# Kernel tuning notes

Hardware: AMD Instinct MI355X
Metric: run time of the kernel (lower is better)

The kernel has to match this reference:

```python
import jax, jax.numpy as jnp
import numpy as np

H, F, E = 1024, 2816, 8   # hidden_size, intermediate_size, num_local_experts
B, S = 2, 2048
TOP_K = 2


def setup_inputs() -> dict:
    key = jax.random.key(0)
    ks = jax.random.split(key, 5)
    scale = 0.02
    return {
        "hidden_states": jax.random.normal(ks[0], (B, S, H), jnp.float32),
        "gate_w": jax.random.normal(ks[1], (E, H), jnp.float32) * scale,
        "w1": jax.random.normal(ks[2], (E, F, H), jnp.float32) * scale,
        "w3": jax.random.normal(ks[3], (E, F, H), jnp.float32) * scale,
        "w2": jax.random.normal(ks[4], (E, H, F), jnp.float32) * scale,
    }


def reference(hidden_states, gate_w, w1, w3, w2):
    b, s, h = hidden_states.shape
    e = gate_w.shape[0]
    T = b * s
    x = hidden_states.reshape(T, h)                      # [T, H]
    router_logits = x @ gate_w.T                         # [T, E]
    probs = jax.nn.softmax(router_logits, axis=-1)
    topw, sel = jax.lax.top_k(probs, TOP_K)              # [T, K]
    topw = topw / jnp.sum(topw, axis=-1, keepdims=True)  # renormalize over top-k
    # dense combine weights [T, E] (equivalent to the per-expert scatter/index_add)
    comb = jnp.zeros((T, e), x.dtype).at[jnp.arange(T)[:, None], sel].add(topw)
    hidden = jax.nn.silu(jnp.einsum('th,efh->etf', x, w1)) * jnp.einsum('th,efh->etf', x, w3)
    y = jnp.einsum('etf,ehf->eth', hidden, w2)           # [E, T, H]
    out = jnp.einsum('eth,te->th', y, comb)              # weighted scatter-combine
    return out.reshape(b, s, h), router_logits
```

## Files before the change

kernel.cpp:

```cpp
#include <hip/hip_runtime.h>
#include <hip/hip_bf16.h>
#include <stdint.h>

#define T_TOK 4096
#define H_DIM 1024
#define F_DIM 2816
#define E_NUM 8

typedef __attribute__((ext_vector_type(8))) __bf16 bf16x8;
typedef __attribute__((ext_vector_type(4))) float floatx4;
typedef __attribute__((address_space(3))) char lds_char;
typedef __attribute__((address_space(1))) const char glb_char;

__device__ __forceinline__ void gload16(const void* g, void* l) {
  __builtin_amdgcn_global_load_lds((glb_char*)g, (lds_char*)l, 16, 0, 0);
}

__device__ __forceinline__ unsigned pack2bf16(float a, float b) {
  unsigned ua = __builtin_bit_cast(unsigned, a);
  unsigned ub = __builtin_bit_cast(unsigned, b);
  ua += 0x7fffu + ((ua >> 16) & 1u);
  ub += 0x7fffu + ((ub >> 16) & 1u);
  return (ua >> 16) | (ub & 0xffff0000u);
}

__device__ __forceinline__ float b2f(unsigned short u) {
  unsigned v = ((unsigned)u) << 16;
  return __builtin_bit_cast(float, v);
}

__device__ __forceinline__ int swz(int row, int colb) {
  return (row * 128 + colb) ^ ((row & 7) << 4);
}

__global__ __launch_bounds__(256) void convert_kernel(
    const float* __restrict__ src, __hip_bfloat16* __restrict__ dst,
    int nchunk8) {
  int i = blockIdx.x * blockDim.x + threadIdx.x;
  const int stride = gridDim.x * blockDim.x;
  for (; i < nchunk8; i += stride) {
    const float4* s = (const float4*)(src + (size_t)i * 8);
    float4 a = s[0], b = s[1];
    uint4 p;
    p.x = pack2bf16(a.x, a.y); p.y = pack2bf16(a.z, a.w);
    p.z = pack2bf16(b.x, b.y); p.w = pack2bf16(b.z, b.w);
    *(uint4*)((char*)dst + (size_t)i * 16) = p;
  }
}

__global__ __launch_bounds__(256) void convert_w13(
    const float* __restrict__ w1, const float* __restrict__ w3,
    __hip_bfloat16* __restrict__ wB) {
  const int e = blockIdx.y;
  const int rho = blockIdx.x * 2 + (threadIdx.x >> 7);
  const int hc = threadIdx.x & 127;
  const int f = ((rho >> 5) << 4) + (rho & 15);
  const float* src = ((rho >> 4) & 1 ? w3 : w1) +
                     ((size_t)e * F_DIM + f) * H_DIM + hc * 8;
  const float4* s = (const float4*)src;
  float4 a = s[0], b = s[1];
  uint4 p;
  p.x = pack2bf16(a.x, a.y); p.y = pack2bf16(a.z, a.w);
  p.z = pack2bf16(b.x, b.y); p.w = pack2bf16(b.z, b.w);
  *(uint4*)((char*)wB + (((size_t)e * (2 * F_DIM) + rho) * H_DIM + hc * 8) * 2)
      = p;
}

__global__ __launch_bounds__(256) void router_kernel(
    const float* __restrict__ x, const float* __restrict__ gate,
    float* __restrict__ logits_out, __hip_bfloat16* __restrict__ xb,
    int* __restrict__ counts, int* __restrict__ idx_list,
    float* __restrict__ wgt_list, int* __restrict__ meta0,
    int* __restrict__ meta1, float* __restrict__ wcomb)
{
  const int wv = threadIdx.x >> 6;
  const int lane = threadIdx.x & 63;
  const int t = blockIdx.x * 4 + wv;

  const float4* xr = (const float4*)(x + (size_t)t * H_DIM);
  const float4* g4 = (const float4*)gate;

  float acc[E_NUM];
#pragma unroll
  for (int e = 0; e < E_NUM; ++e) acc[e] = 0.f;

  unsigned* xbo = (unsigned*)(xb + (size_t)t * H_DIM);
#pragma unroll
  for (int j = 0; j < 4; ++j) {
    int i = j * 64 + lane;
    float4 xv = xr[i];
    uint2 pk;
    pk.x = pack2bf16(xv.x, xv.y);
    pk.y = pack2bf16(xv.z, xv.w);
    *(uint2*)(xbo + i * 2) = pk;
#pragma unroll
    for (int e = 0; e < E_NUM; ++e) {
      float4 gv = g4[e * 256 + i];
      acc[e] += xv.x * gv.x + xv.y * gv.y + xv.z * gv.z + xv.w * gv.w;
    }
  }
#pragma unroll
  for (int off = 32; off > 0; off >>= 1) {
#pragma unroll
    for (int e = 0; e < E_NUM; ++e) acc[e] += __shfl_xor(acc[e], off, 64);
  }

  if (lane == 0) {
#pragma unroll
    for (int e = 0; e < E_NUM; ++e) logits_out[(size_t)t * E_NUM + e] = acc[e];
    int i0 = 0; float v0 = acc[0];
#pragma unroll
    for (int e = 1; e < E_NUM; ++e) if (acc[e] > v0) { v0 = acc[e]; i0 = e; }
    int i1 = -1; float v1 = -1e30f;
#pragma unroll
    for (int e = 0; e < E_NUM; ++e)
      if (e != i0 && acc[e] > v1) { v1 = acc[e]; i1 = e; }
    float p1 = __expf(v1 - v0);
    float w0 = 1.f / (1.f + p1);
    float w1 = p1 / (1.f + p1);
    int pos0 = atomicAdd(&counts[i0], 1);
    idx_list[i0 * T_TOK + pos0] = t;
    wgt_list[i0 * T_TOK + pos0] = w0;
    int pos1 = atomicAdd(&counts[i1], 1);
    idx_list[i1 * T_TOK + pos1] = t;
    wgt_list[i1 * T_TOK + pos1] = w1;
    meta0[t] = (i0 << 16) | pos0;
    meta1[t] = (i1 << 16) | pos1;
    wcomb[t] = w0;
  }
}

__global__ void scan_kernel(const int* __restrict__ counts,
                            int* __restrict__ offsets) {
  if (threadIdx.x == 0) {
    int s = 0;
    for (int e = 0; e < E_NUM; ++e) { offsets[e] = s; s += counts[e]; }
  }
}

__global__ __launch_bounds__(512, 2) void gemm1_kernel(
    const __hip_bfloat16* __restrict__ xb,
    const __hip_bfloat16* __restrict__ wB,
    const int* __restrict__ counts, const int* __restrict__ offsets,
    const int* __restrict__ idx_list, __hip_bfloat16* __restrict__ hidden)
{
  const int e = blockIdx.z;
  const int n_e = counts[e];
  const int tm = blockIdx.y;
  if (n_e == 0 || tm * 256 >= n_e) return;
  const int tn = blockIdx.x;
  const int off_e = offsets[e];

  __shared__ char lds[131072];
  char* sA = lds;
  char* sB = lds + 65536;

  const int tid = threadIdx.x;
  const int lane = tid & 63;
  const int wv = tid >> 6;
  const int wrow = (wv >> 2) * 128;
  const int wcol = (wv & 3) * 64;
  const int csw = ((lane & 7) ^ (lane >> 3)) << 4;
  const int wvb = wv * 1024;

  size_t aoff[4];
#pragma unroll
  for (int i = 0; i < 4; ++i) {
    int r = i * 64 + wv * 8 + (lane >> 3);
    int pos = tm * 256 + r;
    int p = pos < n_e ? pos : n_e - 1;
    aoff[i] = (size_t)idx_list[e * T_TOK + p] * 2048;
  }
  const char* xbp = (const char*)xb;
  const char* wBp =
      (const char*)wB + ((size_t)e * (2 * F_DIM) + tn * 256) * 2048;
  size_t boff[4];
#pragma unroll
  for (int i = 0; i < 4; ++i)
    boff[i] = (size_t)(i * 64 + wv * 8 + (lane >> 3)) * 2048;

  floatx4 acc[8][4];
#pragma unroll
  for (int m = 0; m < 8; ++m)
#pragma unroll
    for (int n = 0; n < 4; ++n)
#pragma unroll
      for (int r = 0; r < 4; ++r) acc[m][n][r] = 0.f;

#define STAGE1(set, kb)                                                \
  do {                                                                 \
    char* dA = sA + (set) * 32768 + wvb;                               \
    char* dB = sB + (set) * 32768 + wvb;                               \
    _Pragma("unroll")                                                  \
    for (int i = 0; i < 4; ++i) {                                      \
      gload16(xbp + aoff[i] + (kb) + csw, dA + i * 8192);              \
      gload16(wBp + boff[i] + (kb) + csw, dB + i * 8192);              \
    }                                                                  \
  } while (0)

  asm volatile("s_waitcnt vmcnt(0)" ::: "memory");
  STAGE1(0, 0);

  int cur = 0;
  for (int kt = 0; kt < H_DIM / 64; ++kt) {
    if (kt < H_DIM / 64 - 1) {
      STAGE1(cur ^ 1, (kt + 1) * 128);
      asm volatile("s_waitcnt vmcnt(8)" ::: "memory");
    } else {
      asm volatile("s_waitcnt vmcnt(0)" ::: "memory");
    }
    __syncthreads();
    const char* rA = sA + cur * 32768;
    const char* rB = sB + cur * 32768;
#pragma unroll
    for (int kk = 0; kk < 2; ++kk) {
      const int colb = kk * 64 + (lane >> 4) * 16;
      bf16x8 af[8], bx[4];
#pragma unroll
      for (int m = 0; m < 8; ++m)
        af[m] = *(const bf16x8*)(rA + swz(wrow + m * 16 + (lane & 15), colb));
#pragma unroll
      for (int n = 0; n < 4; ++n)
        bx[n] = *(const bf16x8*)(rB + swz(wcol + n * 16 + (lane & 15), colb));
#pragma unroll
      for (int m = 0; m < 8; ++m)
#pragma unroll
        for (int n = 0; n < 4; ++n)
          acc[m][n] = __builtin_amdgcn_mfma_f32_16x16x32_bf16(
              af[m], bx[n], acc[m][n], 0, 0, 0);
    }
    __syncthreads();
    cur ^= 1;
  }
#undef STAGE1

  const int fbase = (tn * 8 + (wcol >> 5)) * 16 + (lane & 15);
#pragma unroll
  for (int m = 0; m < 8; ++m) {
#pragma unroll
    for (int r = 0; r < 4; ++r) {
      int pos = tm * 256 + wrow + m * 16 + ((lane >> 4) << 2) + r;
      if (pos < n_e) {
        __hip_bfloat16* hrow = hidden + (size_t)(off_e + pos) * F_DIM;
#pragma unroll
        for (int j = 0; j < 2; ++j) {
          float h1 = acc[m][2 * j][r];
          float h3 = acc[m][2 * j + 1][r];
          float h = (h1 / (1.f + __expf(-h1))) * h3;
          hrow[fbase + j * 16] = __float2bfloat16(h);
        }
      }
    }
  }
}

__global__ __launch_bounds__(256, 2) void gemm2_kernel(
    const __hip_bfloat16* __restrict__ hidden,
    const __hip_bfloat16* __restrict__ w2b,
    const int* __restrict__ counts, const int* __restrict__ offsets,
    __hip_bfloat16* __restrict__ y)
{
  const int e = blockIdx.z;
  const int n_e = counts[e];
  const int tm = blockIdx.y;
  if (n_e == 0 || tm * 128 >= n_e) return;
  const int tn = blockIdx.x;
  const int n0 = tn * 128;
  const int off_e = offsets[e];

  __shared__ char lds[65536];
  char* sA = lds;
  char* sB = lds + 32768;

  const int tid = threadIdx.x;
  const int lane = tid & 63;
  const int wv = tid >> 6;
  const int wrow = (wv >> 1) * 64;
  const int wcol = (wv & 1) * 64;
  const int csw = ((lane & 7) ^ (lane >> 3)) << 4;
  const int wvb = wv * 1024;

  size_t aoff[4], boff[4];
#pragma unroll
  for (int i = 0; i < 4; ++i) {
    int r = i * 32 + wv * 8 + (lane >> 3);
    int pos = tm * 128 + r;
    int p = pos < n_e ? pos : n_e - 1;
    aoff[i] = (size_t)(off_e + p) * (F_DIM * 2);
    boff[i] = ((size_t)e * H_DIM + n0 + r) * (F_DIM * 2);
  }
  const char* hp = (const char*)hidden;
  const char* w2p = (const char*)w2b;

  floatx4 acc[4][4];
#pragma unroll
  for (int m = 0; m < 4; ++m)
#pragma unroll
    for (int n = 0; n < 4; ++n)
#pragma unroll
      for (int r = 0; r < 4; ++r) acc[m][n][r] = 0.f;

#define STAGE2(set, kb)                                                \
  do {                                                                 \
    char* dA = sA + (set) * 16384 + wvb;                               \
    char* dB = sB + (set) * 16384 + wvb;                               \
    _Pragma("unroll")                                                  \
    for (int i = 0; i < 4; ++i) {                                      \
      gload16(hp + aoff[i] + (kb) + csw, dA + i * 4096);               \
      gload16(w2p + boff[i] + (kb) + csw, dB + i * 4096);              \
    }                                                                  \
  } while (0)

  asm volatile("s_waitcnt vmcnt(0)" ::: "memory");
  STAGE2(0, 0);

  int cur = 0;
  for (int kt = 0; kt < F_DIM / 64; ++kt) {
    if (kt < F_DIM / 64 - 1) {
      STAGE2(cur ^ 1, (kt + 1) * 128);
      asm volatile("s_waitcnt vmcnt(8)" ::: "memory");
    } else {
      asm volatile("s_waitcnt vmcnt(0)" ::: "memory");
    }
    __syncthreads();
    const char* rA = sA + cur * 16384;
    const char* rB = sB + cur * 16384;
#pragma unroll
    for (int kk = 0; kk < 2; ++kk) {
      const int colb = kk * 64 + (lane >> 4) * 16;
      bf16x8 af[4], bx[4];
#pragma unroll
      for (int m = 0; m < 4; ++m)
        af[m] = *(const bf16x8*)(rA + swz(wrow + m * 16 + (lane & 15), colb));
#pragma unroll
      for (int n = 0; n < 4; ++n)
        bx[n] = *(const bf16x8*)(rB + swz(wcol + n * 16 + (lane & 15), colb));
#pragma unroll
      for (int m = 0; m < 4; ++m)
#pragma unroll
        for (int n = 0; n < 4; ++n)
          acc[m][n] = __builtin_amdgcn_mfma_f32_16x16x32_bf16(
              af[m], bx[n], acc[m][n], 0, 0, 0);
    }
    __syncthreads();
    cur ^= 1;
  }
#undef STAGE2

#pragma unroll
  for (int m = 0; m < 4; ++m) {
#pragma unroll
    for (int r = 0; r < 4; ++r) {
      int pos = tm * 128 + wrow + m * 16 + ((lane >> 4) << 2) + r;
      if (pos < n_e) {
        __hip_bfloat16* yrow = y + (size_t)(off_e + pos) * H_DIM + n0;
#pragma unroll
        for (int n = 0; n < 4; ++n)
          yrow[wcol + n * 16 + (lane & 15)] = __float2bfloat16(acc[m][n][r]);
      }
    }
  }
}

__global__ __launch_bounds__(256) void combine_kernel(
    const __hip_bfloat16* __restrict__ y, const int* __restrict__ offsets,
    const int* __restrict__ meta0, const int* __restrict__ meta1,
    const float* __restrict__ wcomb, float* __restrict__ out)
{
  const int t = blockIdx.x;
  const int m0 = meta0[t], m1 = meta1[t];
  const float w0 = wcomb[t];
  const float w1 = 1.f - w0;
  const size_t s0 = (size_t)(offsets[m0 >> 16] + (m0 & 0xffff)) * H_DIM;
  const size_t s1 = (size_t)(offsets[m1 >> 16] + (m1 & 0xffff)) * H_DIM;
  const int c = threadIdx.x * 4;
  ushort4 a = *(const ushort4*)(y + s0 + c);
  ushort4 b = *(const ushort4*)(y + s1 + c);
  float4 o;
  o.x = w0 * b2f(a.x) + w1 * b2f(b.x);
  o.y = w0 * b2f(a.y) + w1 * b2f(b.y);
  o.z = w0 * b2f(a.z) + w1 * b2f(b.z);
  o.w = w0 * b2f(a.w) + w1 * b2f(b.w);
  *(float4*)(out + (size_t)t * H_DIM + c) = o;
}

__global__ __launch_bounds__(256) void gemm1_fb(
    const __hip_bfloat16* __restrict__ xb,
    const float* __restrict__ w1, const float* __restrict__ w3,
    const int* __restrict__ counts, const int* __restrict__ offsets,
    const int* __restrict__ idx_list, __hip_bfloat16* __restrict__ hidden)
{
  const int e = blockIdx.z;
  const int n_e = counts[e];
  const int tm = blockIdx.y;
  if (n_e == 0 || tm * 128 >= n_e) return;
  const int tn = blockIdx.x;
  const int f0 = tn * 128;
  const int off_e = offsets[e];

  __shared__ short sA[128 * 64];
  __shared__ short sB1[128 * 64];
  __shared__ short sB3[128 * 64];
  __shared__ int s_row[128];

  const int tid = threadIdx.x;
  if (tid < 128) {
    int pos = tm * 128 + tid;
    int p = pos < n_e ? pos : n_e - 1;
    s_row[tid] = idx_list[e * T_TOK + p];
  }
  const int lane = tid & 63;
  const int wv = tid >> 6;
  const int wrow = (wv >> 1) * 64;
  const int wcol = (wv & 1) * 64;
  const int cc = tid & 7;
  const int rbase = tid >> 3;

  floatx4 acc1[4][4], acc3[4][4];
#pragma unroll
  for (int m = 0; m < 4; ++m)
#pragma unroll
    for (int n = 0; n < 4; ++n)
#pragma unroll
      for (int r = 0; r < 4; ++r) { acc1[m][n][r] = 0.f; acc3[m][n][r] = 0.f; }

  const float* w1e = w1 + (size_t)e * F_DIM * H_DIM + (size_t)f0 * H_DIM;
  const float* w3e = w3 + (size_t)e * F_DIM * H_DIM + (size_t)f0 * H_DIM;

  for (int kt = 0; kt < H_DIM / 64; ++kt) {
    const int k0 = kt * 64;
    __syncthreads();
#pragma unroll
    for (int i = 0; i < 4; ++i) {
      int r = rbase + 32 * i;
      uint4 av = *(const uint4*)(xb + (size_t)s_row[r] * H_DIM + k0 + cc * 8);
      *(uint4*)((char*)sA + swz(r, cc * 16)) = av;
      const float4* p1 = (const float4*)(w1e + (size_t)r * H_DIM + k0 + cc * 8);
      float4 a1 = p1[0], b1 = p1[1];
      uint4 pb1;
      pb1.x = pack2bf16(a1.x, a1.y); pb1.y = pack2bf16(a1.z, a1.w);
      pb1.z = pack2bf16(b1.x, b1.y); pb1.w = pack2bf16(b1.z, b1.w);
      *(uint4*)((char*)sB1 + swz(r, cc * 16)) = pb1;
      const float4* p3 = (const float4*)(w3e + (size_t)r * H_DIM + k0 + cc * 8);
      float4 a3 = p3[0], b3 = p3[1];
      uint4 pb3;
      pb3.x = pack2bf16(a3.x, a3.y); pb3.y = pack2bf16(a3.z, a3.w);
      pb3.z = pack2bf16(b3.x, b3.y); pb3.w = pack2bf16(b3.z, b3.w);
      *(uint4*)((char*)sB3 + swz(r, cc * 16)) = pb3;
    }
    __syncthreads();
#pragma unroll
    for (int kk = 0; kk < 2; ++kk) {
      const int colb = kk * 64 + (lane >> 4) * 16;
      bf16x8 af[4], bf1[4], bf3[4];
#pragma unroll
      for (int m = 0; m < 4; ++m)
        af[m] = *(const bf16x8*)((const char*)sA +
                                 swz(wrow + m * 16 + (lane & 15), colb));
#pragma unroll
      for (int n = 0; n < 4; ++n) {
        bf1[n] = *(const bf16x8*)((const char*)sB1 +
                                  swz(wcol + n * 16 + (lane & 15), colb));
        bf3[n] = *(const bf16x8*)((const char*)sB3 +
                                  swz(wcol + n * 16 + (lane & 15), colb));
      }
#pragma unroll
      for (int m = 0; m < 4; ++m)
#pragma unroll
        for (int n = 0; n < 4; ++n) {
          acc1[m][n] = __builtin_amdgcn_mfma_f32_16x16x32_bf16(
              af[m], bf1[n], acc1[m][n], 0, 0, 0);
          acc3[m][n] = __builtin_amdgcn_mfma_f32_16x16x32_bf16(
              af[m], bf3[n], acc3[m][n], 0, 0, 0);
        }
    }
  }
#pragma unroll
  for (int m = 0; m < 4; ++m) {
#pragma unroll
    for (int r = 0; r < 4; ++r) {
      int rl = wrow + m * 16 + ((lane >> 4) << 2) + r;
      int pos = tm * 128 + rl;
      if (pos < n_e) {
        __hip_bfloat16* hrow = hidden + (size_t)(off_e + pos) * F_DIM + f0;
#pragma unroll
        for (int n = 0; n < 4; ++n) {
          float h1 = acc1[m][n][r];
          float h3 = acc3[m][n][r];
          float h = (h1 / (1.f + __expf(-h1))) * h3;
          hrow[wcol + n * 16 + (lane & 15)] = __float2bfloat16(h);
        }
      }
    }
  }
}

__global__ __launch_bounds__(256) void gemm2_fb(
    const __hip_bfloat16* __restrict__ hidden, const float* __restrict__ w2,
    const int* __restrict__ counts, const int* __restrict__ offsets,
    const int* __restrict__ idx_list, const float* __restrict__ wgt_list,
    float* __restrict__ out)
{
  const int e = blockIdx.z;
  const int n_e = counts[e];
  const int tm = blockIdx.y;
  if (n_e == 0 || tm * 128 >= n_e) return;
  const int tn = blockIdx.x;
  const int n0 = tn * 128;
  const int off_e = offsets[e];

  __shared__ short sA[128 * 64];
  __shared__ short sB[128 * 64];
  __shared__ int s_tok[128];
  __shared__ float s_wgt[128];

  const int tid = threadIdx.x;
  if (tid < 128) {
    int pos = tm * 128 + tid;
    if (pos < n_e) {
      s_tok[tid] = idx_list[e * T_TOK + pos];
      s_wgt[tid] = wgt_list[e * T_TOK + pos];
    } else {
      s_tok[tid] = -1;
      s_wgt[tid] = 0.f;
    }
  }
  const int lane = tid & 63;
  const int wv = tid >> 6;
  const int wrow = (wv >> 1) * 64;
  const int wcol = (wv & 1) * 64;
  const int cc = tid & 7;
  const int rbase = tid >> 3;

  floatx4 acc[4][4];
#pragma unroll
  for (int m = 0; m < 4; ++m)
#pragma unroll
    for (int n = 0; n < 4; ++n)
#pragma unroll
      for (int r = 0; r < 4; ++r) acc[m][n][r] = 0.f;

  const float* w2e = w2 + (size_t)e * H_DIM * F_DIM + (size_t)n0 * F_DIM;

  for (int kt = 0; kt < F_DIM / 64; ++kt) {
    const int k0 = kt * 64;
    __syncthreads();
#pragma unroll
    for (int i = 0; i < 4; ++i) {
      int r = rbase + 32 * i;
      int pos = tm * 128 + r;
      int pr = pos < n_e ? pos : n_e - 1;
      uint4 av = *(const uint4*)(hidden + (size_t)(off_e + pr) * F_DIM +
                                 k0 + cc * 8);
      *(uint4*)((char*)sA + swz(r, cc * 16)) = av;
      const float4* pb = (const float4*)(w2e + (size_t)r * F_DIM + k0 + cc * 8);
      float4 ba = pb[0], bb = pb[1];
      uint4 pk;
      pk.x = pack2bf16(ba.x, ba.y); pk.y = pack2bf16(ba.z, ba.w);
      pk.z = pack2bf16(bb.x, bb.y); pk.w = pack2bf16(bb.z, bb.w);
      *(uint4*)((char*)sB + swz(r, cc * 16)) = pk;
    }
    __syncthreads();
#pragma unroll
    for (int kk = 0; kk < 2; ++kk) {
      const int colb = kk * 64 + (lane >> 4) * 16;
      bf16x8 af[4], bf[4];
#pragma unroll
      for (int m = 0; m < 4; ++m)
        af[m] = *(const bf16x8*)((const char*)sA +
                                 swz(wrow + m * 16 + (lane & 15), colb));
#pragma unroll
      for (int n = 0; n < 4; ++n)
        bf[n] = *(const bf16x8*)((const char*)sB +
                                 swz(wcol + n * 16 + (lane & 15), colb));
#pragma unroll
      for (int m = 0; m < 4; ++m)
#pragma unroll
        for (int n = 0; n < 4; ++n)
          acc[m][n] = __builtin_amdgcn_mfma_f32_16x16x32_bf16(
              af[m], bf[n], acc[m][n], 0, 0, 0);
    }
  }
#pragma unroll
  for (int m = 0; m < 4; ++m) {
#pragma unroll
    for (int r = 0; r < 4; ++r) {
      int rl = wrow + m * 16 + ((lane >> 4) << 2) + r;
      int tok = s_tok[rl];
      if (tok >= 0) {
        float wgt = s_wgt[rl];
        float* orow = out + (size_t)tok * H_DIM + n0;
#pragma unroll
        for (int n = 0; n < 4; ++n)
          atomicAdd(&orow[wcol + n * 16 + (lane & 15)], wgt * acc[m][n][r]);
      }
    }
  }
}

extern "C" void kernel_launch(void* const* d_in, const int* in_sizes, int n_in,
                              void* d_out, int out_size, void* d_ws,
                              size_t ws_size, hipStream_t stream) {
  const float* x = (const float*)d_in[0];
  const float* gate = (const float*)d_in[1];
  const float* w1 = (const float*)d_in[2];
  const float* w3 = (const float*)d_in[3];
  const float* w2 = (const float*)d_in[4];

  float* out = (float*)d_out;
  float* logits = out + (size_t)T_TOK * H_DIM;

  char* ws = (char*)d_ws;
  const size_t o_idx = 256;
  const size_t o_wgt = o_idx + (size_t)E_NUM * T_TOK * 4;
  const size_t o_m0  = o_wgt + (size_t)E_NUM * T_TOK * 4;
  const size_t o_m1  = o_m0 + (size_t)T_TOK * 4;
  const size_t o_wc  = o_m1 + (size_t)T_TOK * 4;
  const size_t o_xb  = o_wc + (size_t)T_TOK * 4;
  const size_t o_hid = o_xb + (size_t)T_TOK * H_DIM * 2;
  const size_t o_wB  = o_hid + (size_t)2 * T_TOK * F_DIM * 2;
  const size_t o_w2b = o_wB + (size_t)E_NUM * 2 * F_DIM * H_DIM * 2;
  const size_t need  = o_w2b + (size_t)E_NUM * H_DIM * F_DIM * 2;

  int* counts = (int*)ws;
  int* offsets = counts + 8;
  int* idx_list = (int*)(ws + o_idx);
  float* wgt_list = (float*)(ws + o_wgt);
  int* meta0 = (int*)(ws + o_m0);
  int* meta1 = (int*)(ws + o_m1);
  float* wcomb = (float*)(ws + o_wc);
  __hip_bfloat16* xb = (__hip_bfloat16*)(ws + o_xb);
  __hip_bfloat16* hidden = (__hip_bfloat16*)(ws + o_hid);

  hipMemsetAsync(counts, 0, 64, stream);

  if (ws_size >= need) {
    __hip_bfloat16* wB = (__hip_bfloat16*)(ws + o_wB);
    __hip_bfloat16* w2b = (__hip_bfloat16*)(ws + o_w2b);
    __hip_bfloat16* y = (__hip_bfloat16*)(ws + o_wB);

    convert_w13<<<dim3(F_DIM, E_NUM), 256, 0, stream>>>(w1, w3, wB);
    convert_kernel<<<2048, 256, 0, stream>>>(
        w2, w2b, E_NUM * F_DIM * H_DIM / 8);
    router_kernel<<<T_TOK / 4, 256, 0, stream>>>(
        x, gate, logits, xb, counts, idx_list, wgt_list, meta0, meta1, wcomb);
    scan_kernel<<<1, 64, 0, stream>>>(counts, offsets);
    gemm1_kernel<<<dim3(2 * F_DIM / 256, T_TOK / 256, E_NUM), 512, 0,
                   stream>>>(xb, wB, counts, offsets, idx_list, hidden);
    gemm2_kernel<<<dim3(H_DIM / 128, T_TOK / 128, E_NUM), 256, 0, stream>>>(
        hidden, w2b, counts, offsets, y);
    combine_kernel<<<T_TOK, 256, 0, stream>>>(y, offsets, meta0, meta1, wcomb,
                                              out);
  } else {
    hipMemsetAsync(out, 0, (size_t)T_TOK * H_DIM * sizeof(float), stream);
    router_kernel<<<T_TOK / 4, 256, 0, stream>>>(
        x, gate, logits, xb, counts, idx_list, wgt_list, meta0, meta1, wcomb);
    scan_kernel<<<1, 64, 0, stream>>>(counts, offsets);
    gemm1_fb<<<dim3(F_DIM / 128, T_TOK / 128, E_NUM), 256, 0, stream>>>(
        xb, w1, w3, counts, offsets, idx_list, hidden);
    gemm2_fb<<<dim3(H_DIM / 128, T_TOK / 128, E_NUM), 256, 0, stream>>>(
        hidden, w2, counts, offsets, idx_list, wgt_list, out);
  }
}
```

Measured before the change: 446.8 us.

## Split-K gemm2 in halves and remap gemm1 block order across experts

gemm2 now splits its F reduction into two halves along a doubled grid z dimension, writing two partial y buffers that the combine kernel sums. This doubles the block count to fill the GPU better, at the cost of extra y traffic and bf16 rounding of each partial. gemm1 linearizes its block index and remaps it so that consecutive blocks hit different experts in a rotated pattern. That is meant to spread work and weight reads across experts and balance early exits. The second y half sits at an offset of 2*T*H in the workspace, which relies on the region aliased over wB being large enough.

Result: no change. 447.2 us (+0.1%).

```diff
diff --git a/kernel.cpp b/kernel.cpp
--- a/kernel.cpp
+++ b/kernel.cpp
@@ -144,11 +144,14 @@
     const int* __restrict__ counts, const int* __restrict__ offsets,
     const int* __restrict__ idx_list, __hip_bfloat16* __restrict__ hidden)
 {
-  const int e = blockIdx.z;
+  const int L = blockIdx.x + 22 * (blockIdx.y + 16 * blockIdx.z);
+  const int k = L & 7;
+  const int r = L >> 3;
+  const int tn = r >> 4;
+  const int tm = r & 15;
+  const int e = (k - tn) & 7;
   const int n_e = counts[e];
-  const int tm = blockIdx.y;
   if (n_e == 0 || tm * 256 >= n_e) return;
-  const int tn = blockIdx.x;
   const int off_e = offsets[e];
 
   __shared__ char lds[131072];
@@ -166,8 +169,8 @@
   size_t aoff[4];
 #pragma unroll
   for (int i = 0; i < 4; ++i) {
-    int r = i * 64 + wv * 8 + (lane >> 3);
-    int pos = tm * 256 + r;
+    int rr = i * 64 + wv * 8 + (lane >> 3);
+    int pos = tm * 256 + rr;
     int p = pos < n_e ? pos : n_e - 1;
     aoff[i] = (size_t)idx_list[e * T_TOK + p] * 2048;
   }
@@ -185,7 +188,7 @@
 #pragma unroll
     for (int n = 0; n < 4; ++n)
 #pragma unroll
-      for (int r = 0; r < 4; ++r) acc[m][n][r] = 0.f;
+      for (int q = 0; q < 4; ++q) acc[m][n][q] = 0.f;
 
 #define STAGE1(set, kb)                                                \
   do {                                                                 \
@@ -238,14 +241,14 @@
 #pragma unroll
   for (int m = 0; m < 8; ++m) {
 #pragma unroll
-    for (int r = 0; r < 4; ++r) {
-      int pos = tm * 256 + wrow + m * 16 + ((lane >> 4) << 2) + r;
+    for (int q = 0; q < 4; ++q) {
+      int pos = tm * 256 + wrow + m * 16 + ((lane >> 4) << 2) + q;
       if (pos < n_e) {
         __hip_bfloat16* hrow = hidden + (size_t)(off_e + pos) * F_DIM;
 #pragma unroll
         for (int j = 0; j < 2; ++j) {
-          float h1 = acc[m][2 * j][r];
-          float h3 = acc[m][2 * j + 1][r];
+          float h1 = acc[m][2 * j][q];
+          float h3 = acc[m][2 * j + 1][q];
           float h = (h1 / (1.f + __expf(-h1))) * h3;
           hrow[fbase + j * 16] = __float2bfloat16(h);
         }
@@ -260,13 +263,15 @@
     const int* __restrict__ counts, const int* __restrict__ offsets,
     __hip_bfloat16* __restrict__ y)
 {
-  const int e = blockIdx.z;
+  const int e = blockIdx.z & 7;
+  const int kh = blockIdx.z >> 3;
+  const int tm = blockIdx.y;
+  const int tn = blockIdx.x;
   const int n_e = counts[e];
-  const int tm = blockIdx.y;
   if (n_e == 0 || tm * 128 >= n_e) return;
-  const int tn = blockIdx.x;
   const int n0 = tn * 128;
   const int off_e = offsets[e];
+  const int kbase = kh * (F_DIM);
 
   __shared__ char lds[65536];
   char* sA = lds;
@@ -283,11 +288,11 @@
   size_t aoff[4], boff[4];
 #pragma unroll
   for (int i = 0; i < 4; ++i) {
-    int r = i * 32 + wv * 8 + (lane >> 3);
-    int pos = tm * 128 + r;
+    int rr = i * 32 + wv * 8 + (lane >> 3);
+    int pos = tm * 128 + rr;
     int p = pos < n_e ? pos : n_e - 1;
     aoff[i] = (size_t)(off_e + p) * (F_DIM * 2);
-    boff[i] = ((size_t)e * H_DIM + n0 + r) * (F_DIM * 2);
+    boff[i] = ((size_t)e * H_DIM + n0 + rr) * (F_DIM * 2);
   }
   const char* hp = (const char*)hidden;
   const char* w2p = (const char*)w2b;
@@ -298,7 +303,7 @@
 #pragma unroll
     for (int n = 0; n < 4; ++n)
 #pragma unroll
-      for (int r = 0; r < 4; ++r) acc[m][n][r] = 0.f;
+      for (int q = 0; q < 4; ++q) acc[m][n][q] = 0.f;
 
 #define STAGE2(set, kb)                                                \
   do {                                                                 \
@@ -312,12 +317,13 @@
   } while (0)
 
   asm volatile("s_waitcnt vmcnt(0)" ::: "memory");
-  STAGE2(0, 0);
+  STAGE2(0, kbase);
 
   int cur = 0;
-  for (int kt = 0; kt < F_DIM / 64; ++kt) {
-    if (kt < F_DIM / 64 - 1) {
-      STAGE2(cur ^ 1, (kt + 1) * 128);
+  const int NKT = F_DIM / 64 / 2;
+  for (int kt = 0; kt < NKT; ++kt) {
+    if (kt < NKT - 1) {
+      STAGE2(cur ^ 1, kbase + (kt + 1) * 128);
       asm volatile("s_waitcnt vmcnt(8)" ::: "memory");
     } else {
       asm volatile("s_waitcnt vmcnt(0)" ::: "memory");
@@ -347,16 +353,17 @@
   }
 #undef STAGE2
 
+  __hip_bfloat16* yh = y + (size_t)kh * (2 * T_TOK) * H_DIM;
 #pragma unroll
   for (int m = 0; m < 4; ++m) {
 #pragma unroll
-    for (int r = 0; r < 4; ++r) {
-      int pos = tm * 128 + wrow + m * 16 + ((lane >> 4) << 2) + r;
+    for (int q = 0; q < 4; ++q) {
+      int pos = tm * 128 + wrow + m * 16 + ((lane >> 4) << 2) + q;
       if (pos < n_e) {
-        __hip_bfloat16* yrow = y + (size_t)(off_e + pos) * H_DIM + n0;
+        __hip_bfloat16* yrow = yh + (size_t)(off_e + pos) * H_DIM + n0;
 #pragma unroll
         for (int n = 0; n < 4; ++n)
-          yrow[wcol + n * 16 + (lane & 15)] = __float2bfloat16(acc[m][n][r]);
+          yrow[wcol + n * 16 + (lane & 15)] = __float2bfloat16(acc[m][n][q]);
       }
     }
   }
@@ -373,14 +380,17 @@
   const float w1 = 1.f - w0;
   const size_t s0 = (size_t)(offsets[m0 >> 16] + (m0 & 0xffff)) * H_DIM;
   const size_t s1 = (size_t)(offsets[m1 >> 16] + (m1 & 0xffff)) * H_DIM;
+  const size_t HB = (size_t)(2 * T_TOK) * H_DIM;
   const int c = threadIdx.x * 4;
-  ushort4 a = *(const ushort4*)(y + s0 + c);
-  ushort4 b = *(const ushort4*)(y + s1 + c);
+  ushort4 a0 = *(const ushort4*)(y + s0 + c);
+  ushort4 a1 = *(const ushort4*)(y + HB + s0 + c);
+  ushort4 b0 = *(const ushort4*)(y + s1 + c);
+  ushort4 b1 = *(const ushort4*)(y + HB + s1 + c);
   float4 o;
-  o.x = w0 * b2f(a.x) + w1 * b2f(b.x);
-  o.y = w0 * b2f(a.y) + w1 * b2f(b.y);
-  o.z = w0 * b2f(a.z) + w1 * b2f(b.z);
-  o.w = w0 * b2f(a.w) + w1 * b2f(b.w);
+  o.x = w0 * (b2f(a0.x) + b2f(a1.x)) + w1 * (b2f(b0.x) + b2f(b1.x));
+  o.y = w0 * (b2f(a0.y) + b2f(a1.y)) + w1 * (b2f(b0.y) + b2f(b1.y));
+  o.z = w0 * (b2f(a0.z) + b2f(a1.z)) + w1 * (b2f(b0.z) + b2f(b1.z));
+  o.w = w0 * (b2f(a0.w) + b2f(a1.w)) + w1 * (b2f(b0.w) + b2f(b1.w));
   *(float4*)(out + (size_t)t * H_DIM + c) = o;
 }
 
@@ -422,7 +432,7 @@
 #pragma unroll
     for (int n = 0; n < 4; ++n)
 #pragma unroll
-      for (int r = 0; r < 4; ++r) { acc1[m][n][r] = 0.f; acc3[m][n][r] = 0.f; }
+      for (int q = 0; q < 4; ++q) { acc1[m][n][q] = 0.f; acc3[m][n][q] = 0.f; }
 
   const float* w1e = w1 + (size_t)e * F_DIM * H_DIM + (size_t)f0 * H_DIM;
   const float* w3e = w3 + (size_t)e * F_DIM * H_DIM + (size_t)f0 * H_DIM;
@@ -432,21 +442,21 @@
     __syncthreads();
 #pragma unroll
     for (int i = 0; i < 4; ++i) {
-      int r = rbase + 32 * i;
-      uint4 av = *(const uint4*)(xb + (size_t)s_row[r] * H_DIM + k0 + cc * 8);
-      *(uint4*)((char*)sA + swz(r, cc * 16)) = av;
-      const float4* p1 = (const float4*)(w1e + (size_t)r * H_DIM + k0 + cc * 8);
+      int rr = rbase + 32 * i;
+      uint4 av = *(const uint4*)(xb + (size_t)s_row[rr] * H_DIM + k0 + cc * 8);
+      *(uint4*)((char*)sA + swz(rr, cc * 16)) = av;
+      const float4* p1 = (const float4*)(w1e + (size_t)rr * H_DIM + k0 + cc * 8);
       float4 a1 = p1[0], b1 = p1[1];
       uint4 pb1;
       pb1.x = pack2bf16(a1.x, a1.y); pb1.y = pack2bf16(a1.z, a1.w);
       pb1.z = pack2bf16(b1.x, b1.y); pb1.w = pack2bf16(b1.z, b1.w);
-      *(uint4*)((char*)sB1 + swz(r, cc * 16)) = pb1;
-      const float4* p3 = (const float4*)(w3e + (size_t)r * H_DIM + k0 + cc * 8);
+      *(uint4*)((char*)sB1 + swz(rr, cc * 16)) = pb1;
+      const float4* p3 = (const float4*)(w3e + (size_t)rr * H_DIM + k0 + cc * 8);
       float4 a3 = p3[0], b3 = p3[1];
       uint4 pb3;
       pb3.x = pack2bf16(a3.x, a3.y); pb3.y = pack2bf16(a3.z, a3.w);
       pb3.z = pack2bf16(b3.x, b3.y); pb3.w = pack2bf16(b3.z, b3.w);
-      *(uint4*)((char*)sB3 + swz(r, cc * 16)) = pb3;
+      *(uint4*)((char*)sB3 + swz(rr, cc * 16)) = pb3;
     }
     __syncthreads();
 #pragma unroll
@@ -478,15 +488,15 @@
 #pragma unroll
   for (int m = 0; m < 4; ++m) {
 #pragma unroll
-    for (int r = 0; r < 4; ++r) {
-      int rl = wrow + m * 16 + ((lane >> 4) << 2) + r;
+    for (int q = 0; q < 4; ++q) {
+      int rl = wrow + m * 16 + ((lane >> 4) << 2) + q;
       int pos = tm * 128 + rl;
       if (pos < n_e) {
         __hip_bfloat16* hrow = hidden + (size_t)(off_e + pos) * F_DIM + f0;
 #pragma unroll
         for (int n = 0; n < 4; ++n) {
-          float h1 = acc1[m][n][r];
-          float h3 = acc3[m][n][r];
+          float h1 = acc1[m][n][q];
+          float h3 = acc3[m][n][q];
           float h = (h1 / (1.f + __expf(-h1))) * h3;
           hrow[wcol + n * 16 + (lane & 15)] = __float2bfloat16(h);
         }
@@ -538,7 +548,7 @@
 #pragma unroll
     for (int n = 0; n < 4; ++n)
 #pragma unroll
-      for (int r = 0; r < 4; ++r) acc[m][n][r] = 0.f;
+      for (int q = 0; q < 4; ++q) acc[m][n][q] = 0.f;
 
   const float* w2e = w2 + (size_t)e * H_DIM * F_DIM + (size_t)n0 * F_DIM;
 
@@ -547,18 +557,18 @@
     __syncthreads();
 #pragma unroll
     for (int i = 0; i < 4; ++i) {
-      int r = rbase + 32 * i;
-      int pos = tm * 128 + r;
+      int rr = rbase + 32 * i;
+      int pos = tm * 128 + rr;
       int pr = pos < n_e ? pos : n_e - 1;
       uint4 av = *(const uint4*)(hidden + (size_t)(off_e + pr) * F_DIM +
                                  k0 + cc * 8);
-      *(uint4*)((char*)sA + swz(r, cc * 16)) = av;
-      const float4* pb = (const float4*)(w2e + (size_t)r * F_DIM + k0 + cc * 8);
+      *(uint4*)((char*)sA + swz(rr, cc * 16)) = av;
+      const float4* pb = (const float4*)(w2e + (size_t)rr * F_DIM + k0 + cc * 8);
       float4 ba = pb[0], bb = pb[1];
       uint4 pk;
       pk.x = pack2bf16(ba.x, ba.y); pk.y = pack2bf16(ba.z, ba.w);
       pk.z = pack2bf16(bb.x, bb.y); pk.w = pack2bf16(bb.z, bb.w);
-      *(uint4*)((char*)sB + swz(r, cc * 16)) = pk;
+      *(uint4*)((char*)sB + swz(rr, cc * 16)) = pk;
     }
     __syncthreads();
 #pragma unroll
@@ -584,15 +594,15 @@
 #pragma unroll
   for (int m = 0; m < 4; ++m) {
 #pragma unroll
-    for (int r = 0; r < 4; ++r) {
-      int rl = wrow + m * 16 + ((lane >> 4) << 2) + r;
+    for (int q = 0; q < 4; ++q) {
+      int rl = wrow + m * 16 + ((lane >> 4) << 2) + q;
       int tok = s_tok[rl];
       if (tok >= 0) {
         float wgt = s_wgt[rl];
         float* orow = out + (size_t)tok * H_DIM + n0;
 #pragma unroll
         for (int n = 0; n < 4; ++n)
-          atomicAdd(&orow[wcol + n * 16 + (lane & 15)], wgt * acc[m][n][r]);
+          atomicAdd(&orow[wcol + n * 16 + (lane & 15)], wgt * acc[m][n][q]);
       }
     }
   }
@@ -645,9 +655,9 @@
     router_kernel<<<T_TOK / 4, 256, 0, stream>>>(
         x, gate, logits, xb, counts, idx_list, wgt_list, meta0, meta1, wcomb);
     scan_kernel<<<1, 64, 0, stream>>>(counts, offsets);
-    gemm1_kernel<<<dim3(2 * F_DIM / 256, T_TOK / 256, E_NUM), 512, 0,
-                   stream>>>(xb, wB, counts, offsets, idx_list, hidden);
-    gemm2_kernel<<<dim3(H_DIM / 128, T_TOK / 128, E_NUM), 256, 0, stream>>>(
+    gemm1_kernel<<<dim3(22, 16, E_NUM), 512, 0, stream>>>(
+        xb, wB, counts, offsets, idx_list, hidden);
+    gemm2_kernel<<<dim3(8, 32, 2 * E_NUM), 256, 0, stream>>>(
         hidden, w2b, counts, offsets, y);
     combine_kernel<<<T_TOK, 256, 0, stream>>>(y, offsets, meta0, meta1, wcomb,
                                               out);
```
